# Performance work log

Hardware: AMD Instinct MI355X
Metric: run time of the kernel (lower is better)

The kernel has to match this reference:

```python
import jax, jax.numpy as jnp
import numpy as np

B, C, M, N = 16, 512, 256, 4096

def setup_inputs() -> dict:
    key = jax.random.key(0)
    k1, k2, k3 = jax.random.split(key, 3)
    x = jax.random.normal(k1, (B, C, N), dtype=jnp.float32)
    # Conv1d(C, M, 1, bias=False) weight: [M, C] (kernel size 1 squeezed)
    Wk = jax.random.normal(k2, (M, C), dtype=jnp.float32) * (1.0 / np.sqrt(C))
    # Conv1d(M, C, 1, bias=False) weight: [C, M]
    Wv = jax.random.normal(k3, (C, M), dtype=jnp.float32) * (1.0 / np.sqrt(M))
    return {"x": x, "Wk": Wk, "Wv": Wv}

def reference(x, Wk, Wv):
    # attn = M_k(x): 1x1 conv == matmul over channel dim -> [B, M, N]
    attn = jnp.einsum("mc,bcn->bmn", Wk, x)
    # softmax over sequence dim N
    attn = jax.nn.softmax(attn, axis=2)
    # L1 normalization over memory-unit (channel) dim M
    attn = attn / (1e-9 + attn.sum(axis=1, keepdims=True))
    # out = M_v(attn): [B, C, N]
    out = jnp.einsum("cm,bmn->bcn", Wv, attn)
    return x + out
```

## Files before the change

### kernel.cpp

```cpp
#include <hip/hip_runtime.h>
#include <hip/hip_bf16.h>

#define Bdim 16
#define Cdim 512
#define Mdim 256
#define Ndim 4096

typedef short bf16x8 __attribute__((ext_vector_type(8)));
typedef float f32x4 __attribute__((ext_vector_type(4)));
typedef unsigned short us8 __attribute__((ext_vector_type(8)));
typedef unsigned short us4 __attribute__((ext_vector_type(4)));

__device__ __forceinline__ unsigned short f2b(float f) {
  union { float f; unsigned int u; } v; v.f = f;
  return (unsigned short)((v.u + 0x8000u) >> 16);
}
__device__ __forceinline__ float b2f(unsigned short h) {
  union { unsigned int u; float f; } v; v.u = ((unsigned int)h) << 16;
  return v.f;
}

__global__ __launch_bounds__(256) void k0_convert(
    const float* __restrict__ gWk, const float* __restrict__ gWv,
    unsigned short* __restrict__ oWk, unsigned short* __restrict__ oWv) {
  const int i = (blockIdx.x * 256 + threadIdx.x) * 4;
  f32x4 a = *reinterpret_cast<const f32x4*>(gWk + i);
  f32x4 b = *reinterpret_cast<const f32x4*>(gWv + i);
  us4 ha, hb;
#pragma unroll
  for (int j = 0; j < 4; ++j) { ha[j] = f2b(a[j]); hb[j] = f2b(b[j]); }
  *reinterpret_cast<us4*>(oWk + i) = ha;
  *reinterpret_cast<us4*>(oWv + i) = hb;
}

__global__ __launch_bounds__(256) void k1_gemm1(
    const float* __restrict__ gx, const unsigned short* __restrict__ gWkB,
    unsigned short* __restrict__ gS) {
  __shared__ unsigned short Wk_s[64 * 64];
  __shared__ unsigned short xT_s[64 * 72];
  const int t = threadIdx.x;
  const int b = blockIdx.z;
  const int m0 = blockIdx.y * 64;
  const int n0 = blockIdx.x * 64;
  const int w = t >> 6;
  const int lane = t & 63;
  const int lr = lane & 15;
  const int lg = lane >> 4;
  const int wm = (w >> 1) * 32;
  const int wn = (w & 1) * 32;

  f32x4 acc[2][2] = {};
  const float* xb = gx + (size_t)b * Cdim * Ndim + n0;

  const int nq = t & 15;
  const int cq = t >> 4;
  const int wrow = lane >> 3;
  const int wchk = (lane & 7) ^ (wrow & 7);

  for (int ck = 0; ck < Cdim; ck += 64) {
    {
#pragma unroll
      for (int j = 0; j < 2; ++j) {
        const unsigned short* gsrc =
            gWkB + (size_t)(m0 + w * 16 + j * 8 + wrow) * Cdim + ck + wchk * 8;
        __builtin_amdgcn_global_load_lds(
            (const __attribute__((address_space(1))) unsigned int*)gsrc,
            (__attribute__((address_space(3))) unsigned int*)&Wk_s[(w * 16 + j * 8) * 64],
            16, 0, 0);
      }
    }
    {
      const int cb = cq * 4;
      const float* src = xb + (size_t)(ck + cb) * Ndim + nq * 4;
      f32x4 v[4];
#pragma unroll
      for (int j = 0; j < 4; ++j)
        v[j] = *reinterpret_cast<const f32x4*>(src + (size_t)j * Ndim);
      char* dst = reinterpret_cast<char*>(xT_s) + ((cb * 2) ^ ((nq & 7) << 4));
#pragma unroll
      for (int k = 0; k < 4; ++k) {
        us4 h;
#pragma unroll
        for (int j = 0; j < 4; ++j)
          h[j] = (unsigned short)(__float_as_uint(v[j][k]) >> 16);
        *reinterpret_cast<us4*>(dst + (nq * 4 + k) * 144) = h;
      }
    }
    __syncthreads();
#pragma unroll
    for (int kk = 0; kk < 64; kk += 32) {
      bf16x8 af[2], bfr[2];
#pragma unroll
      for (int mi = 0; mi < 2; ++mi) {
        const int rm = wm + mi * 16 + lr;
        af[mi] = *reinterpret_cast<const bf16x8*>(
            reinterpret_cast<const char*>(Wk_s) +
            rm * 128 + ((kk * 2 + lg * 16) ^ ((rm & 7) << 4)));
      }
#pragma unroll
      for (int ni = 0; ni < 2; ++ni) {
        const int rn = wn + ni * 16 + lr;
        bfr[ni] = *reinterpret_cast<const bf16x8*>(
            reinterpret_cast<const char*>(xT_s) +
            rn * 144 + ((kk * 2 + lg * 16) ^ (((rn >> 2) & 7) << 4)));
      }
#pragma unroll
      for (int mi = 0; mi < 2; ++mi)
#pragma unroll
        for (int ni = 0; ni < 2; ++ni)
          acc[mi][ni] = __builtin_amdgcn_mfma_f32_16x16x32_bf16(
              af[mi], bfr[ni], acc[mi][ni], 0, 0, 0);
    }
    __syncthreads();
  }
  unsigned short* Sb = gS + ((size_t)b * Mdim + m0 + wm) * Ndim + n0 + wn;
#pragma unroll
  for (int mi = 0; mi < 2; ++mi)
#pragma unroll
    for (int ni = 0; ni < 2; ++ni)
#pragma unroll
      for (int r = 0; r < 4; ++r) {
        int m = mi * 16 + lg * 4 + r;
        int n = ni * 16 + lr;
        Sb[(size_t)m * Ndim + n] = f2b(acc[mi][ni][r]);
      }
}

__global__ __launch_bounds__(256) void k2_rowstats(
    const unsigned short* __restrict__ gS, float* __restrict__ stats) {
  const int m = blockIdx.x;
  const int b = blockIdx.y;
  const unsigned short* row = gS + ((size_t)b * Mdim + m) * Ndim;
  const int t = threadIdx.x;
  const int w = t >> 6;
  float s = 0.f;
#pragma unroll
  for (int i = 0; i < 2; ++i) {
    us8 u = *reinterpret_cast<const us8*>(row + i * 2048 + t * 8);
#pragma unroll
    for (int j = 0; j < 8; ++j) s += __expf(b2f(u[j]));
  }
#pragma unroll
  for (int o = 32; o > 0; o >>= 1) s += __shfl_xor(s, o, 64);
  __shared__ float redsum[4];
  if ((t & 63) == 0) redsum[w] = s;
  __syncthreads();
  if (t == 0) {
    float tot = redsum[0] + redsum[1] + redsum[2] + redsum[3];
    stats[(size_t)b * Mdim + m] = 1.0f / tot;
  }
}

#define K3_PAD 264

__global__ __launch_bounds__(256) void k3_norm(
    const unsigned short* __restrict__ gS, const float* __restrict__ stats,
    unsigned short* __restrict__ gPT) {
  __shared__ unsigned short P_s[64 * K3_PAD];
  __shared__ float cs[4][64];
  __shared__ float rtot[64];
  const int b = blockIdx.y;
  const int n0 = blockIdx.x * 64;
  const int t = threadIdx.x;
  const int w = t >> 6;
  const int l = t & 63;
  const unsigned short* Sb = gS + ((size_t)b * Mdim + w * 64) * Ndim + n0 + l;
  const float* stb = stats + (size_t)b * Mdim + w * 64;
  float acc = 0.f;
#pragma unroll
  for (int i8 = 0; i8 < 8; ++i8) {
    us8 pk;
#pragma unroll
    for (int jj = 0; jj < 8; ++jj) {
      const int mi = i8 * 8 + jj;
      float p = __expf(b2f(Sb[(size_t)mi * Ndim])) * stb[mi];
      acc += p;
      pk[jj] = f2b(p);
    }
    *reinterpret_cast<us8*>(&P_s[l * K3_PAD + w * 64 + i8 * 8]) = pk;
  }
  cs[w][l] = acc;
  __syncthreads();
  if (w == 0) rtot[l] = 1.0f / (1e-9f + cs[0][l] + cs[1][l] + cs[2][l] + cs[3][l]);
  __syncthreads();
  const int mo = (t & 31) * 8;
#pragma unroll
  for (int j = 0; j < 8; ++j) {
    const int n = (t >> 5) + j * 8;
    const float rc = rtot[n];
    us8 pv = *reinterpret_cast<const us8*>(&P_s[n * K3_PAD + mo]);
    us8 o;
#pragma unroll
    for (int q = 0; q < 8; ++q) o[q] = f2b(b2f(pv[q]) * rc);
    *reinterpret_cast<us8*>(gPT + ((size_t)b * Ndim + n0 + n) * Mdim + mo) = o;
  }
}

#define K4_P 136

__global__ __launch_bounds__(256) void k4_gemm2(
    const float* __restrict__ gx, const unsigned short* __restrict__ gWvB,
    const unsigned short* __restrict__ gPT, float* __restrict__ gout) {
  __shared__ unsigned short Wv_s[128 * K4_P];
  __shared__ unsigned short PT_s[64 * K4_P];
  const int t = threadIdx.x;
  const int b = blockIdx.z;
  const int c0 = blockIdx.y * 128;
  const int n0 = blockIdx.x * 64;
  const int w = t >> 6;
  const int lane = t & 63;
  const int lr = lane & 15;
  const int lg = lane >> 4;
  const int wc = (w >> 1) * 64;
  const int wn = (w & 1) * 32;

  f32x4 acc[4][2] = {};

  for (int ck = 0; ck < Mdim; ck += 128) {
#pragma unroll
    for (int i = 0; i < 8; ++i) {
      int q = i * 256 + t;
      int r = q >> 4;
      int mq = (q & 15) * 8;
      us8 u = *reinterpret_cast<const us8*>(gWvB + (size_t)(c0 + r) * Mdim + ck + mq);
      *reinterpret_cast<us8*>(&Wv_s[r * K4_P + mq]) = u;
    }
#pragma unroll
    for (int i = 0; i < 4; ++i) {
      int q = i * 256 + t;
      int r = q >> 4;
      int mq = (q & 15) * 8;
      us8 u = *reinterpret_cast<const us8*>(gPT + ((size_t)b * Ndim + n0 + r) * Mdim + ck + mq);
      *reinterpret_cast<us8*>(&PT_s[r * K4_P + mq]) = u;
    }
    __syncthreads();
#pragma unroll
    for (int kk = 0; kk < 128; kk += 32) {
      bf16x8 af[4], bfr[2];
#pragma unroll
      for (int ci = 0; ci < 4; ++ci)
        af[ci] = *reinterpret_cast<const bf16x8*>(
            &Wv_s[(wc + ci * 16 + lr) * K4_P + kk + lg * 8]);
#pragma unroll
      for (int ni = 0; ni < 2; ++ni)
        bfr[ni] = *reinterpret_cast<const bf16x8*>(
            &PT_s[(wn + ni * 16 + lr) * K4_P + kk + lg * 8]);
#pragma unroll
      for (int ci = 0; ci < 4; ++ci)
#pragma unroll
        for (int ni = 0; ni < 2; ++ni)
          acc[ci][ni] = __builtin_amdgcn_mfma_f32_16x16x32_bf16(
              af[ci], bfr[ni], acc[ci][ni], 0, 0, 0);
    }
    __syncthreads();
  }
#pragma unroll
  for (int ci = 0; ci < 4; ++ci)
#pragma unroll
    for (int ni = 0; ni < 2; ++ni)
#pragma unroll
      for (int r = 0; r < 4; ++r) {
        int c = c0 + wc + ci * 16 + lg * 4 + r;
        int n = n0 + wn + ni * 16 + lr;
        size_t idx = ((size_t)b * Cdim + c) * Ndim + n;
        gout[idx] = gx[idx] + acc[ci][ni][r];
      }
}

extern "C" void kernel_launch(void* const* d_in, const int* in_sizes, int n_in,
                              void* d_out, int out_size, void* d_ws, size_t ws_size,
                              hipStream_t stream) {
  const float* x = (const float*)d_in[0];
  const float* Wk = (const float*)d_in[1];
  const float* Wv = (const float*)d_in[2];
  float* out = (float*)d_out;

  unsigned short* S = (unsigned short*)d_ws;
  unsigned short* PT = S + (size_t)Bdim * Mdim * Ndim;
  float* stats = (float*)(PT + (size_t)Bdim * Ndim * Mdim);
  unsigned short* WkB = (unsigned short*)(stats + Bdim * Mdim);
  unsigned short* WvB = WkB + Mdim * Cdim;

  k0_convert<<<dim3((Mdim * Cdim) / 1024), 256, 0, stream>>>(Wk, Wv, WkB, WvB);
  k1_gemm1<<<dim3(Ndim / 64, Mdim / 64, Bdim), 256, 0, stream>>>(x, WkB, S);
  k2_rowstats<<<dim3(Mdim, Bdim), 256, 0, stream>>>(S, stats);
  k3_norm<<<dim3(Ndim / 64, Bdim), 256, 0, stream>>>(S, stats, PT);
  k4_gemm2<<<dim3(Ndim / 64, Cdim / 128, Bdim), 256, 0, stream>>>(x, WvB, PT, out);
}
```

Baseline: 128.6 us.

## Pre-transpose x to bf16 in a separate kernel and enlarge GEMM1 tiles

Adds a kernel that converts x to bf16 and transposes it to [B,N,C] in workspace, so GEMM1 reads contiguous bf16 rows instead of reconverting fp32 x once per M tile. GEMM1 now uses a 128x64 tile with a K step of 128 and padded LDS rows in place of the XOR swizzle, and plain vector loads in place of global_load_lds. The extra pass writes and rereads 64MB of bf16 data and adds a launch, in exchange for halving the redundant reads of x across M tiles.

```diff
diff --git a/kernel.cpp b/kernel.cpp
--- a/kernel.cpp
+++ b/kernel.cpp
@@ -33,96 +33,118 @@
   *reinterpret_cast<us4*>(oWv + i) = hb;
 }
 
+__global__ __launch_bounds__(256) void k0x_transpose(
+    const float* __restrict__ gx, unsigned short* __restrict__ gxT) {
+  __shared__ unsigned short T_s[64 * 264];
+  const int t = threadIdx.x;
+  const int b = blockIdx.z;
+  const int n0 = blockIdx.x * 64;
+  const int c0 = blockIdx.y * 256;
+  const int nq = t & 15;
+  const int cq = t >> 4;
+  const float* xb = gx + (size_t)b * Cdim * Ndim + n0;
+#pragma unroll
+  for (int p = 0; p < 4; ++p) {
+    const int cb = (cq + p * 16) * 4;
+    const float* src = xb + (size_t)(c0 + cb) * Ndim + nq * 4;
+    f32x4 v[4];
+#pragma unroll
+    for (int j = 0; j < 4; ++j)
+      v[j] = *reinterpret_cast<const f32x4*>(src + (size_t)j * Ndim);
+    char* dst = reinterpret_cast<char*>(T_s) + ((cb * 2) ^ ((nq & 7) << 4));
+#pragma unroll
+    for (int k = 0; k < 4; ++k) {
+      us4 h;
+#pragma unroll
+      for (int j = 0; j < 4; ++j)
+        h[j] = (unsigned short)(__float_as_uint(v[j][k]) >> 16);
+      *reinterpret_cast<us4*>(dst + (nq * 4 + k) * 528) = h;
+    }
+  }
+  __syncthreads();
+  unsigned short* dstg = gxT + ((size_t)b * Ndim + n0) * Cdim + c0;
+#pragma unroll
+  for (int pass = 0; pass < 4; ++pass) {
+    const int row = pass * 16 + (t >> 4);
+    const int sw = ((row >> 2) & 7) << 4;
+#pragma unroll
+    for (int jj = 0; jj < 2; ++jj) {
+      const int chunk = (t & 15) + jj * 16;
+      us8 vv = *reinterpret_cast<const us8*>(
+          reinterpret_cast<const char*>(T_s) + row * 528 + ((chunk * 16) ^ sw));
+      *reinterpret_cast<us8*>(dstg + (size_t)row * Cdim + chunk * 8) = vv;
+    }
+  }
+}
+
+#define K1_P 136
+
 __global__ __launch_bounds__(256) void k1_gemm1(
-    const float* __restrict__ gx, const unsigned short* __restrict__ gWkB,
+    const unsigned short* __restrict__ gWkB, const unsigned short* __restrict__ gxT,
     unsigned short* __restrict__ gS) {
-  __shared__ unsigned short Wk_s[64 * 64];
-  __shared__ unsigned short xT_s[64 * 72];
+  __shared__ unsigned short Wk_s[128 * K1_P];
+  __shared__ unsigned short xT_s[64 * K1_P];
   const int t = threadIdx.x;
   const int b = blockIdx.z;
-  const int m0 = blockIdx.y * 64;
+  const int m0 = blockIdx.y * 128;
   const int n0 = blockIdx.x * 64;
   const int w = t >> 6;
   const int lane = t & 63;
   const int lr = lane & 15;
   const int lg = lane >> 4;
-  const int wm = (w >> 1) * 32;
+  const int wm = (w >> 1) * 64;
   const int wn = (w & 1) * 32;
 
-  f32x4 acc[2][2] = {};
-  const float* xb = gx + (size_t)b * Cdim * Ndim + n0;
-
-  const int nq = t & 15;
-  const int cq = t >> 4;
-  const int wrow = lane >> 3;
-  const int wchk = (lane & 7) ^ (wrow & 7);
-
-  for (int ck = 0; ck < Cdim; ck += 64) {
-    {
-#pragma unroll
-      for (int j = 0; j < 2; ++j) {
-        const unsigned short* gsrc =
-            gWkB + (size_t)(m0 + w * 16 + j * 8 + wrow) * Cdim + ck + wchk * 8;
-        __builtin_amdgcn_global_load_lds(
-            (const __attribute__((address_space(1))) unsigned int*)gsrc,
-            (__attribute__((address_space(3))) unsigned int*)&Wk_s[(w * 16 + j * 8) * 64],
-            16, 0, 0);
-      }
-    }
-    {
-      const int cb = cq * 4;
-      const float* src = xb + (size_t)(ck + cb) * Ndim + nq * 4;
-      f32x4 v[4];
-#pragma unroll
-      for (int j = 0; j < 4; ++j)
-        v[j] = *reinterpret_cast<const f32x4*>(src + (size_t)j * Ndim);
-      char* dst = reinterpret_cast<char*>(xT_s) + ((cb * 2) ^ ((nq & 7) << 4));
-#pragma unroll
-      for (int k = 0; k < 4; ++k) {
-        us4 h;
-#pragma unroll
-        for (int j = 0; j < 4; ++j)
-          h[j] = (unsigned short)(__float_as_uint(v[j][k]) >> 16);
-        *reinterpret_cast<us4*>(dst + (nq * 4 + k) * 144) = h;
-      }
+  f32x4 acc[4][2] = {};
+
+  for (int ck = 0; ck < Cdim; ck += 128) {
+#pragma unroll
+    for (int i = 0; i < 8; ++i) {
+      int q = i * 256 + t;
+      int r = q >> 4;
+      int mq = (q & 15) * 8;
+      us8 u = *reinterpret_cast<const us8*>(gWkB + (size_t)(m0 + r) * Cdim + ck + mq);
+      *reinterpret_cast<us8*>(&Wk_s[r * K1_P + mq]) = u;
+    }
+#pragma unroll
+    for (int i = 0; i < 4; ++i) {
+      int q = i * 256 + t;
+      int r = q >> 4;
+      int mq = (q & 15) * 8;
+      us8 u = *reinterpret_cast<const us8*>(gxT + ((size_t)b * Ndim + n0 + r) * Cdim + ck + mq);
+      *reinterpret_cast<us8*>(&xT_s[r * K1_P + mq]) = u;
     }
     __syncthreads();
 #pragma unroll
-    for (int kk = 0; kk < 64; kk += 32) {
-      bf16x8 af[2], bfr[2];
-#pragma unroll
-      for (int mi = 0; mi < 2; ++mi) {
-        const int rm = wm + mi * 16 + lr;
-        af[mi] = *reinterpret_cast<const bf16x8*>(
-            reinterpret_cast<const char*>(Wk_s) +
-            rm * 128 + ((kk * 2 + lg * 16) ^ ((rm & 7) << 4)));
-      }
-#pragma unroll
-      for (int ni = 0; ni < 2; ++ni) {
-        const int rn = wn + ni * 16 + lr;
+    for (int kk = 0; kk < 128; kk += 32) {
+      bf16x8 af[4], bfr[2];
+#pragma unroll
+      for (int ci = 0; ci < 4; ++ci)
+        af[ci] = *reinterpret_cast<const bf16x8*>(
+            &Wk_s[(wm + ci * 16 + lr) * K1_P + kk + lg * 8]);
+#pragma unroll
+      for (int ni = 0; ni < 2; ++ni)
         bfr[ni] = *reinterpret_cast<const bf16x8*>(
-            reinterpret_cast<const char*>(xT_s) +
-            rn * 144 + ((kk * 2 + lg * 16) ^ (((rn >> 2) & 7) << 4)));
-      }
-#pragma unroll
-      for (int mi = 0; mi < 2; ++mi)
+            &xT_s[(wn + ni * 16 + lr) * K1_P + kk + lg * 8]);
+#pragma unroll
+      for (int ci = 0; ci < 4; ++ci)
 #pragma unroll
         for (int ni = 0; ni < 2; ++ni)
-          acc[mi][ni] = __builtin_amdgcn_mfma_f32_16x16x32_bf16(
-              af[mi], bfr[ni], acc[mi][ni], 0, 0, 0);
+          acc[ci][ni] = __builtin_amdgcn_mfma_f32_16x16x32_bf16(
+              af[ci], bfr[ni], acc[ci][ni], 0, 0, 0);
     }
     __syncthreads();
   }
   unsigned short* Sb = gS + ((size_t)b * Mdim + m0 + wm) * Ndim + n0 + wn;
 #pragma unroll
-  for (int mi = 0; mi < 2; ++mi)
+  for (int ci = 0; ci < 4; ++ci)
 #pragma unroll
     for (int ni = 0; ni < 2; ++ni)
 #pragma unroll
       for (int r = 0; r < 4; ++r) {
-        int m = mi * 16 + lg * 4 + r;
+        int m = ci * 16 + lg * 4 + r;
         int n = ni * 16 + lr;
-        Sb[(size_t)m * Ndim + n] = f2b(acc[mi][ni][r]);
+        Sb[(size_t)m * Ndim + n] = f2b(acc[ci][ni][r]);
       }
 }
 
@@ -280,9 +302,11 @@
   float* stats = (float*)(PT + (size_t)Bdim * Ndim * Mdim);
   unsigned short* WkB = (unsigned short*)(stats + Bdim * Mdim);
   unsigned short* WvB = WkB + Mdim * Cdim;
+  unsigned short* xT = WvB + Cdim * Mdim;
 
   k0_convert<<<dim3((Mdim * Cdim) / 1024), 256, 0, stream>>>(Wk, Wv, WkB, WvB);
-  k1_gemm1<<<dim3(Ndim / 64, Mdim / 64, Bdim), 256, 0, stream>>>(x, WkB, S);
+  k0x_transpose<<<dim3(Ndim / 64, Cdim / 256, Bdim), 256, 0, stream>>>(x, xT);
+  k1_gemm1<<<dim3(Ndim / 64, Mdim / 128, Bdim), 256, 0, stream>>>(WkB, xT, S);
   k2_rowstats<<<dim3(Mdim, Bdim), 256, 0, stream>>>(S, stats);
   k3_norm<<<dim3(Ndim / 64, Bdim), 256, 0, stream>>>(S, stats, PT);
   k4_gemm2<<<dim3(Ndim / 64, Cdim / 128, Bdim), 256, 0, stream>>>(x, WvB, PT, out);
```

Result: slower. 160.6 us (+24.9%).
